# Optimization experiments

Measured on AMD Instinct MI355X. Metric: run time of the kernel, lower is better.

The kernel has to match this reference:

```python
import jax, jax.numpy as jnp
import numpy as np

EMBED_DIM = 1024
NUM_HEADS = 16
HEAD_DIM = EMBED_DIM // NUM_HEADS
LN_EPS = 1e-5


def setup_inputs() -> dict:
    key = jax.random.key(0)
    ks = jax.random.split(key, 12)
    B, SQ, SKV, E = 2, 1024, 4096, EMBED_DIM
    s = 1.0 / np.sqrt(E)
    return {
        "query": jax.random.normal(ks[0], (B, SQ, E), jnp.float32),
        "key_value": jax.random.normal(ks[1], (B, SKV, E), jnp.float32),
        "key_value_mask": jax.random.randint(ks[2], (B, SKV), 0, 2, jnp.int32),
        "Wq": jax.random.normal(ks[3], (E, E), jnp.float32) * s,
        "bq": jnp.zeros((E,), jnp.float32),
        "Wk": jax.random.normal(ks[4], (E, E), jnp.float32) * s,
        "bk": jnp.zeros((E,), jnp.float32),
        "Wv": jax.random.normal(ks[5], (E, E), jnp.float32) * s,
        "bv": jnp.zeros((E,), jnp.float32),
        "Wo": jax.random.normal(ks[6], (E, E), jnp.float32) * s,
        "bo": jnp.zeros((E,), jnp.float32),
        "ln_gamma": jnp.ones((E,), jnp.float32),
        "ln_beta": jnp.zeros((E,), jnp.float32),
    }


def reference(query, key_value, key_value_mask, Wq, bq, Wk, bk, Wv, bv, Wo, bo, ln_gamma, ln_beta):
    B, SQ, E = query.shape
    SKV = key_value.shape[1]
    H, D = NUM_HEADS, HEAD_DIM
    # projections (dropout is eval-mode identity)
    q = (query @ Wq.T + bq).reshape(B, SQ, H, D).transpose(0, 2, 1, 3)      # b h sq d
    k = (key_value @ Wk.T + bk).reshape(B, SKV, H, D).transpose(0, 2, 1, 3)  # b h skv d
    v = (key_value @ Wv.T + bv).reshape(B, SKV, H, D).transpose(0, 2, 1, 3)
    scale = jnp.sqrt(jnp.asarray(D, q.dtype))
    scores = jnp.einsum('bhqd,bhkd->bhqk', q, k) / scale                     # b h sq skv
    mask = (key_value_mask != 0)[:, None, None, :]                           # b 1 1 skv
    scores = jnp.where(mask, scores, jnp.asarray(-jnp.inf, scores.dtype))
    attn = jax.nn.softmax(scores, axis=-1)
    out = jnp.einsum('bhqk,bhkd->bhqd', attn, v)
    out = out.transpose(0, 2, 1, 3).reshape(B, SQ, E)
    out = out @ Wo.T + bo
    # post-LN residual
    x = query + out
    mu = jnp.mean(x, axis=-1, keepdims=True)
    var = jnp.mean(jnp.square(x - mu), axis=-1, keepdims=True)
    return (x - mu) * jax.lax.rsqrt(var + LN_EPS) * ln_gamma + ln_beta
```

## Files before the change

kernel.cpp:

```cpp
#include <hip/hip_runtime.h>
#include <cstdint>


typedef __bf16 bf16x8_t  __attribute__((ext_vector_type(8)));
typedef float  f32x4_t   __attribute__((ext_vector_type(4)));
typedef float  f32x16_t  __attribute__((ext_vector_type(16)));

#define E_DIM 1024
#define NH    16
#define HD    64
#define SCALE_L2E 0.1803368804f

__device__ __forceinline__ unsigned short f32_bf16(float f) {
    union { float f; unsigned int u; } v; v.f = f;
    unsigned int u = v.u;
    unsigned int r = (u + 0x7fffu + ((u >> 16) & 1u)) >> 16;
    return (unsigned short)r;
}

__device__ __forceinline__ unsigned pack_bf16(float a, float b) {
    __bf16 x = (__bf16)a, y = (__bf16)b;
    unsigned short ux = __builtin_bit_cast(unsigned short, x);
    unsigned short uy = __builtin_bit_cast(unsigned short, y);
    return (unsigned)ux | ((unsigned)uy << 16);
}

__device__ __forceinline__ void gld16(const unsigned short* g, unsigned short* l) {
    __builtin_amdgcn_global_load_lds(
        (const __attribute__((address_space(1))) unsigned int*)g,
        (__attribute__((address_space(3))) unsigned int*)l, 16, 0, 0);
}

__device__ __forceinline__ bf16x8_t ld16g(const unsigned short* p) {
    union { uint4 u; bf16x8_t f; } v;
    v.u = *reinterpret_cast<const uint4*>(p);
    return v.f;
}

__global__ void cast_all(const float* __restrict__ q, const float* __restrict__ kv,
                         const float* __restrict__ wq, const float* __restrict__ wk,
                         const float* __restrict__ wv, const float* __restrict__ wo,
                         unsigned short* __restrict__ Xq, unsigned short* __restrict__ Xkv,
                         unsigned short* __restrict__ Wqb, unsigned short* __restrict__ Wkb,
                         unsigned short* __restrict__ Wvb, unsigned short* __restrict__ Wob,
                         const int* __restrict__ msk, float* __restrict__ Sub) {
    __shared__ int red[4];
    if (blockIdx.x >= 14336) {
        int b = blockIdx.x - 14336, t = threadIdx.x;
        int s = 0;
#pragma unroll
        for (int k = 0; k < 16; k++) s += (msk[b * 4096 + k * 256 + t] != 0);
#pragma unroll
        for (int off = 32; off >= 1; off >>= 1) s += __shfl_xor(s, off, 64);
        if ((t & 63) == 0) red[t >> 6] = s;
        __syncthreads();
        if (t == 0)
            Sub[b] = (float)(4096 - (red[0] + red[1] + red[2] + red[3]));
        return;
    }
    long i = (long)blockIdx.x * 256 + threadIdx.x;
    const float* src; unsigned short* dst; long off;
    if (i < 2621440) {
        if (i < 524288) { src = q;  dst = Xq;  off = i; }
        else            { src = kv; dst = Xkv; off = i - 524288; }
    } else {
        long j = i - 2621440;
        int w = (int)(j >> 18); off = j & 262143;
        src = (w == 0) ? wq : (w == 1) ? wk : (w == 2) ? wv : wo;
        dst = (w == 0) ? Wqb : (w == 1) ? Wkb : (w == 2) ? Wvb : Wob;
    }
    float4 v = reinterpret_cast<const float4*>(src)[off];
    ushort4 o;
    o.x = f32_bf16(v.x); o.y = f32_bf16(v.y);
    o.z = f32_bf16(v.z); o.w = f32_bf16(v.w);
    reinterpret_cast<ushort4*>(dst)[off] = o;
}

#define BK 64

__global__ __launch_bounds__(256) void gemm_qkv(
    const unsigned short* __restrict__ Xq,
    const unsigned short* __restrict__ Xkv,
    const unsigned short* __restrict__ Wqb,
    const unsigned short* __restrict__ Wkb,
    const unsigned short* __restrict__ Wvb,
    const float* __restrict__ bq,
    const float* __restrict__ bk,
    const float* __restrict__ bv,
    unsigned short* __restrict__ Qout,
    unsigned short* __restrict__ Kout,
    unsigned short* __restrict__ Vout,
    const int* __restrict__ kvm)
{
    __shared__ __align__(16) unsigned short As[128 * BK];
    __shared__ __align__(16) unsigned short Bs[128 * BK];
    int bid  = blockIdx.x;
    int tid  = threadIdx.x;
    int lane = tid & 63;
    int wvu  = __builtin_amdgcn_readfirstlane(tid >> 6);
    int l15  = lane & 15, quad = lane >> 4, x7 = l15 & 7;

    if (bid < 1024) {
        int xcd  = bid & 7;
        int j    = bid >> 3;
        int mt   = xcd * 8 + (j >> 4);
        int sel  = j & 15;
        int isV  = sel >= 8;
        int m0   = mt * 128;
        int n0   = (sel & 7) * 128;
        const unsigned short* W = isV ? Wvb : Wkb;
        const float* bias = isV ? bv : bk;
        int wm   = ((tid >> 6) >> 1) * 64, wn = ((tid >> 6) & 1) * 64;

        f32x4_t acc[4][4];
#pragma unroll
        for (int i = 0; i < 4; i++)
#pragma unroll
            for (int jj = 0; jj < 4; jj++) acc[i][jj] = (f32x4_t)(0.f);

        for (int k0 = 0; k0 < 1024; k0 += BK) {
            __syncthreads();
#pragma unroll
            for (int i = 0; i < 4; i++) {
                int s = (i * 4 + wvu) * 64 + lane;
                int row = s >> 3, pcol = ((s & 7) ^ (row & 7)) << 3;
                gld16(&Xkv[(long)(m0 + row) * 1024 + k0 + pcol], &As[(i * 4 + wvu) * 512]);
                gld16(&W[(long)(n0 + row) * 1024 + k0 + pcol], &Bs[(i * 4 + wvu) * 512]);
            }
            __syncthreads();
            const char* Ab = (const char*)As;
            const char* Bb = (const char*)Bs;
#pragma unroll
            for (int ks = 0; ks < 2; ks++) {
                int pos = (((ks << 2) + quad) ^ x7) << 4;
                bf16x8_t af[4], bf[4];
#pragma unroll
                for (int mi = 0; mi < 4; mi++)
                    af[mi] = *reinterpret_cast<const bf16x8_t*>(
                        Ab + (wm + mi * 16 + l15) * 128 + pos);
#pragma unroll
                for (int ni = 0; ni < 4; ni++)
                    bf[ni] = *reinterpret_cast<const bf16x8_t*>(
                        Bb + (wn + ni * 16 + l15) * 128 + pos);
#pragma unroll
                for (int mi = 0; mi < 4; mi++)
#pragma unroll
                    for (int ni = 0; ni < 4; ni++)
                        acc[mi][ni] = __builtin_amdgcn_mfma_f32_16x16x32_bf16(
                            af[mi], bf[ni], acc[mi][ni], 0, 0, 0);
            }
        }
        int4 mk[4];
#pragma unroll
        for (int mi = 0; mi < 4; mi++) {
            int mg0 = m0 + wm + mi * 16 + quad * 4;
            mk[mi] = *reinterpret_cast<const int4*>(&kvm[mg0]);
        }
        if (!isV) {
#pragma unroll
            for (int mi = 0; mi < 4; mi++)
#pragma unroll
                for (int ni = 0; ni < 4; ni++) {
                    int n = n0 + wn + ni * 16 + l15;
                    float bvv = bias[n];
                    int h = n >> 6, d = n & 63;
#pragma unroll
                    for (int r = 0; r < 4; r++) {
                        int mg = m0 + wm + mi * 16 + quad * 4 + r;
                        int b = mg >> 12, s = mg & 4095;
                        unsigned short val = (&mk[mi].x)[r]
                            ? f32_bf16(acc[mi][ni][r] + bvv) : (unsigned short)0;
                        Kout[(((b * NH + h) << 12) + s) * HD + d] = val;
                    }
                }
        } else {
#pragma unroll
            for (int mi = 0; mi < 4; mi++)
#pragma unroll
                for (int ni = 0; ni < 4; ni++) {
                    int n = n0 + wn + ni * 16 + l15;
                    float bvv = bias[n];
                    int h = n >> 6, d = n & 63;
                    int mg0 = m0 + wm + mi * 16 + quad * 4;
                    int b = mg0 >> 12, s = mg0 & 4095;
                    ushort4 w;
                    w.x = mk[mi].x ? f32_bf16(acc[mi][ni][0] + bvv) : (unsigned short)0;
                    w.y = mk[mi].y ? f32_bf16(acc[mi][ni][1] + bvv) : (unsigned short)0;
                    w.z = mk[mi].z ? f32_bf16(acc[mi][ni][2] + bvv) : (unsigned short)0;
                    w.w = mk[mi].w ? f32_bf16(acc[mi][ni][3] + bvv) : (unsigned short)0;
                    *reinterpret_cast<ushort4*>(
                        &Vout[(((b * NH + h) * HD + d) << 12) + s]) = w;
                }
        }
    } else {
        int t    = bid - 1024;
        int xcd  = bid & 7;
        int j    = t >> 3;
        int mt   = xcd * 4 + (j >> 3);
        int m0   = mt * 64;
        int n0   = (j & 7) * 128;
        int wm   = ((tid >> 6) >> 1) * 32, wn = ((tid >> 6) & 1) * 64;

        f32x4_t acc[2][4];
#pragma unroll
        for (int i = 0; i < 2; i++)
#pragma unroll
            for (int jj = 0; jj < 4; jj++) acc[i][jj] = (f32x4_t)(0.f);

        for (int k0 = 0; k0 < 1024; k0 += BK) {
            __syncthreads();
#pragma unroll
            for (int i = 0; i < 2; i++) {
                int s = (i * 4 + wvu) * 64 + lane;
                int row = s >> 3, pcol = ((s & 7) ^ (row & 7)) << 3;
                gld16(&Xq[(long)(m0 + row) * 1024 + k0 + pcol], &As[(i * 4 + wvu) * 512]);
            }
#pragma unroll
            for (int i = 0; i < 4; i++) {
                int s = (i * 4 + wvu) * 64 + lane;
                int row = s >> 3, pcol = ((s & 7) ^ (row & 7)) << 3;
                gld16(&Wqb[(long)(n0 + row) * 1024 + k0 + pcol], &Bs[(i * 4 + wvu) * 512]);
            }
            __syncthreads();
            const char* Ab = (const char*)As;
            const char* Bb = (const char*)Bs;
#pragma unroll
            for (int ks = 0; ks < 2; ks++) {
                int pos = (((ks << 2) + quad) ^ x7) << 4;
                bf16x8_t af[2], bf[4];
#pragma unroll
                for (int mi = 0; mi < 2; mi++)
                    af[mi] = *reinterpret_cast<const bf16x8_t*>(
                        Ab + (wm + mi * 16 + l15) * 128 + pos);
#pragma unroll
                for (int ni = 0; ni < 4; ni++)
                    bf[ni] = *reinterpret_cast<const bf16x8_t*>(
                        Bb + (wn + ni * 16 + l15) * 128 + pos);
#pragma unroll
                for (int mi = 0; mi < 2; mi++)
#pragma unroll
                    for (int ni = 0; ni < 4; ni++)
                        acc[mi][ni] = __builtin_amdgcn_mfma_f32_16x16x32_bf16(
                            af[mi], bf[ni], acc[mi][ni], 0, 0, 0);
            }
        }
#pragma unroll
        for (int mi = 0; mi < 2; mi++)
#pragma unroll
            for (int ni = 0; ni < 4; ni++) {
                int n = n0 + wn + ni * 16 + l15;
                float bvq = bq[n];
                int h = n >> 6, d = n & 63;
#pragma unroll
                for (int r = 0; r < 4; r++) {
                    int mg = m0 + wm + mi * 16 + quad * 4 + r;
                    int b = mg >> 10, s = mg & 1023;
                    Qout[(((b * NH + h) << 10) + s) * HD + d] =
                        f32_bf16((acc[mi][ni][r] + bvq) * SCALE_L2E);
                }
            }
    }
}

__global__ __launch_bounds__(256) void gemm_oproj(
    const unsigned short* __restrict__ A,
    const unsigned short* __restrict__ W,
    const float* __restrict__ bias,
    const float* __restrict__ resid,
    float* __restrict__ xout)
{
    __shared__ __align__(16) unsigned short As[32 * BK];
    __shared__ __align__(16) unsigned short Bs[64 * BK];
    int tid  = threadIdx.x;
    int m0   = blockIdx.y * 32;
    int n0   = blockIdx.x * 64;
    int lane = tid & 63;
    int wvu  = __builtin_amdgcn_readfirstlane(tid >> 6);
    int l15  = lane & 15, quad = lane >> 4, x7 = l15 & 7;
    int wn   = (tid >> 6) * 16;

    f32x4_t acc[2];
    acc[0] = (f32x4_t)(0.f); acc[1] = (f32x4_t)(0.f);

    for (int k0 = 0; k0 < 1024; k0 += BK) {
        __syncthreads();
        {
            int s = wvu * 64 + lane;
            int row = s >> 3, pcol = ((s & 7) ^ (row & 7)) << 3;
            gld16(&A[(long)(m0 + row) * 1024 + k0 + pcol], &As[wvu * 512]);
        }
#pragma unroll
        for (int i = 0; i < 2; i++) {
            int s = (i * 4 + wvu) * 64 + lane;
            int row = s >> 3, pcol = ((s & 7) ^ (row & 7)) << 3;
            gld16(&W[(long)(n0 + row) * 1024 + k0 + pcol], &Bs[(i * 4 + wvu) * 512]);
        }
        __syncthreads();
        const char* Ab = (const char*)As;
        const char* Bb = (const char*)Bs;
#pragma unroll
        for (int ks = 0; ks < 2; ks++) {
            int pos = (((ks << 2) + quad) ^ x7) << 4;
            bf16x8_t af[2], bf;
#pragma unroll
            for (int mi = 0; mi < 2; mi++)
                af[mi] = *reinterpret_cast<const bf16x8_t*>(
                    Ab + (mi * 16 + l15) * 128 + pos);
            bf = *reinterpret_cast<const bf16x8_t*>(
                Bb + (wn + l15) * 128 + pos);
#pragma unroll
            for (int mi = 0; mi < 2; mi++)
                acc[mi] = __builtin_amdgcn_mfma_f32_16x16x32_bf16(
                    af[mi], bf, acc[mi], 0, 0, 0);
        }
    }
    int n = n0 + wn + l15;
    float bv = bias[n];
#pragma unroll
    for (int mi = 0; mi < 2; mi++)
#pragma unroll
        for (int r = 0; r < 4; r++) {
            int mg = m0 + mi * 16 + quad * 4 + r;
            xout[mg * 1024 + n] = acc[mi][r] + bv + resid[mg * 1024 + n];
        }
}

__global__ __launch_bounds__(512, 4) void attn_kernel(
    const unsigned short* __restrict__ Q,
    const unsigned short* __restrict__ K,
    const unsigned short* __restrict__ VT,
    float* __restrict__ Osc,
    float* __restrict__ Lsc)
{
    __shared__ __align__(16) union {
        struct { unsigned short Kb[2][4096]; unsigned short Vb[2][4096]; } st;
        struct { float OL[4][2048]; float ls[128]; } mg;
    } sm;

    int tid  = threadIdx.x;
    int lane = tid & 63;
    int w    = tid >> 6;
    int wvu  = __builtin_amdgcn_readfirstlane(w);
    int l31  = lane & 31, hw = lane >> 5;
    int qsub = w & 3, kvsub = w >> 2;

    int bid  = blockIdx.x;
    int xcd  = bid & 7, gidx = bid >> 3;
    int bh   = xcd * 4 + (gidx & 3);
    int rest = gidx >> 2;
    int q0   = (rest & 7) * 128;
    int bhalf = rest >> 3;

    const unsigned short* Kb = K + ((long)bh * 4096 + bhalf * 2048) * HD;
    const unsigned short* Vb = VT + (long)bh * HD * 4096 + bhalf * 2048;
    const unsigned short* Qb = Q + ((long)bh * 1024 + q0) * HD;

    bf16x8_t qfr[4];
#pragma unroll
    for (int ks = 0; ks < 4; ks++)
        qfr[ks] = ld16g(Qb + (qsub * 32 + l31) * HD + ks * 16 + hw * 8);

    f32x16_t oacc[2];
    oacc[0] = (f32x16_t)(0.f); oacc[1] = (f32x16_t)(0.f);
    float l_run = 0.f;

    auto stage = [&](int kt, int bufi) {
        int s = wvu * 64 + lane;
        int row = s >> 3, pc = ((s & 7) ^ (row & 7)) << 3;
        gld16(&Kb[(long)(kt * 64 + row) * HD + pc], &sm.st.Kb[bufi][wvu * 512]);
        gld16(&Vb[(long)row * 4096 + kt * 64 + pc], &sm.st.Vb[bufi][wvu * 512]);
    };

    const char* Kc = (const char*)sm.st.Kb;
    const char* Vc = (const char*)sm.st.Vb;

    stage(0, 0);
#pragma unroll 2
    for (int kt = 0; kt < 32; kt++) {
        __syncthreads();
        if (kt + 1 < 32) stage(kt + 1, (kt + 1) & 1);
        int bo = (kt & 1) * 8192;

        f32x16_t sa = (f32x16_t)(0.f);
        int krow = kvsub * 32 + l31;
        __builtin_amdgcn_s_setprio(1);
#pragma unroll
        for (int ks = 0; ks < 4; ks++) {
            int phys = (ks * 2 + hw) ^ (krow & 7);
            bf16x8_t kf = *reinterpret_cast<const bf16x8_t*>(
                Kc + bo + krow * 128 + phys * 16);
            sa = __builtin_amdgcn_mfma_f32_32x32x16_bf16(kf, qfr[ks], sa, 0, 0, 0);
        }
        __builtin_amdgcn_s_setprio(0);

        float pv[16];
#pragma unroll
        for (int r = 0; r < 16; r++) {
            float e;
            asm("v_exp_f32 %0, %1" : "=v"(e) : "v"(sa[r]));
            pv[r] = e;
        }
        float s0 = (pv[0] + pv[1]) + (pv[2] + pv[3]);
        float s1 = (pv[4] + pv[5]) + (pv[6] + pv[7]);
        float s2 = (pv[8] + pv[9]) + (pv[10] + pv[11]);
        float s3 = (pv[12] + pv[13]) + (pv[14] + pv[15]);
        l_run += (s0 + s1) + (s2 + s3);
        unsigned pku[8];
#pragma unroll
        for (int s4 = 0; s4 < 4; s4++) {
            pku[s4 * 2 + 0] = pack_bf16(pv[s4 * 4 + 0], pv[s4 * 4 + 1]);
            pku[s4 * 2 + 1] = pack_bf16(pv[s4 * 4 + 2], pv[s4 * 4 + 3]);
        }

        __builtin_amdgcn_s_setprio(1);
#pragma unroll
        for (int ks2 = 0; ks2 < 2; ks2++) {
            unsigned x0 = pku[(ks2 * 2) * 2 + 0];
            unsigned x1 = pku[(ks2 * 2) * 2 + 1];
            unsigned z0 = pku[(ks2 * 2 + 1) * 2 + 0];
            unsigned z1 = pku[(ks2 * 2 + 1) * 2 + 1];
            asm("v_permlane32_swap_b32 %0, %1" : "+v"(x0), "+v"(z0));
            asm("v_permlane32_swap_b32 %0, %1" : "+v"(x1), "+v"(z1));
            union { uint4 u; bf16x8_t f; } bw;
            bw.u.x = x0; bw.u.y = x1; bw.u.z = z0; bw.u.w = z1;
            int c = kvsub * 4 + ks2 * 2 + hw;
#pragma unroll
            for (int ds = 0; ds < 2; ds++) {
                int vrow = ds * 32 + l31;
                int phys = c ^ (vrow & 7);
                bf16x8_t va = *reinterpret_cast<const bf16x8_t*>(
                    Vc + bo + vrow * 128 + phys * 16);
                oacc[ds] = __builtin_amdgcn_mfma_f32_32x32x16_bf16(
                    va, bw.f, oacc[ds], 0, 0, 0);
            }
        }
        __builtin_amdgcn_s_setprio(0);
    }

    l_run += __shfl_xor(l_run, 32, 64);
    __syncthreads();
    if (kvsub == 1) {
        float* OL = sm.mg.OL[qsub];
#pragma unroll
        for (int ds = 0; ds < 2; ds++)
#pragma unroll
            for (int r = 0; r < 16; r++) {
                int d = ds * 32 + (r & 3) + 8 * (r >> 2) + 4 * hw;
                OL[d * 32 + l31] = oacc[ds][r];
            }
        if (hw == 0) sm.mg.ls[qsub * 32 + l31] = l_run;
    }
    __syncthreads();
    if (kvsub == 0) {
        const float* OL = sm.mg.OL[qsub];
        int q = q0 + qsub * 32 + l31;
        long obase = (((long)bhalf * 32 + bh) * 64) * 1024;
#pragma unroll
        for (int ds = 0; ds < 2; ds++)
#pragma unroll
            for (int r = 0; r < 16; r++) {
                int d = ds * 32 + (r & 3) + 8 * (r >> 2) + 4 * hw;
                Osc[obase + (long)d * 1024 + q] = oacc[ds][r] + OL[d * 32 + l31];
            }
        if (hw == 0)
            Lsc[((long)bhalf * 32 + bh) * 1024 + q] = l_run + sm.mg.ls[qsub * 32 + l31];
    }
}

__global__ __launch_bounds__(256) void attn_merge(
    const float* __restrict__ Osc, const float* __restrict__ Lsc,
    const float* __restrict__ Sub, unsigned short* __restrict__ AO)
{
    __shared__ unsigned short T[64 * 66];
    int t = threadIdx.x, w = t >> 6, lane = t & 63;
    int bh = blockIdx.y, b = bh >> 4, h = bh & 15;
    int q0 = blockIdx.x * 64;
    int q = q0 + lane;

    float ls = Lsc[(long)bh * 1024 + q]
             + Lsc[(long)(32 + bh) * 1024 + q] - Sub[b];
    float inv = __builtin_amdgcn_rcpf(ls);
    inv = inv * (2.f - ls * inv);

#pragma unroll
    for (int dd = 0; dd < 16; dd++) {
        int d = w * 16 + dd;
        long base = (long)bh * 64 * 1024 + (long)d * 1024 + q;
        float o = Osc[base] + Osc[base + 32l * 64 * 1024];
        T[lane * 66 + d] = f32_bf16(o * inv);
    }
    __syncthreads();
    int q2 = t >> 2, c16 = (t & 3) * 16;
    unsigned ov[8];
#pragma unroll
    for (int j = 0; j < 8; j++)
        ov[j] = *reinterpret_cast<const unsigned*>(&T[q2 * 66 + c16 + j * 2]);
    unsigned short* dst = &AO[((long)(b * 1024 + q0 + q2)) * E_DIM + h * HD + c16];
    reinterpret_cast<uint4*>(dst)[0] = make_uint4(ov[0], ov[1], ov[2], ov[3]);
    reinterpret_cast<uint4*>(dst)[1] = make_uint4(ov[4], ov[5], ov[6], ov[7]);
}

__global__ __launch_bounds__(256) void ln_kernel(
    const float* __restrict__ x, const float* __restrict__ g,
    const float* __restrict__ be, float* __restrict__ out)
{
    __shared__ float red[8];
    int row = blockIdx.x, tid = threadIdx.x;
    float4 v = reinterpret_cast<const float4*>(x)[row * 256 + tid];
    float s  = v.x + v.y + v.z + v.w;
    float sq = v.x * v.x + v.y * v.y + v.z * v.z + v.w * v.w;
#pragma unroll
    for (int off = 32; off >= 1; off >>= 1) {
        s  += __shfl_xor(s,  off, 64);
        sq += __shfl_xor(sq, off, 64);
    }
    if ((tid & 63) == 0) { red[tid >> 6] = s; red[4 + (tid >> 6)] = sq; }
    __syncthreads();
    s  = red[0] + red[1] + red[2] + red[3];
    sq = red[4] + red[5] + red[6] + red[7];
    float mu  = s * (1.f / 1024.f);
    float var = sq * (1.f / 1024.f) - mu * mu;
    float rs  = rsqrtf(var + 1e-5f);
    int c = tid * 4;
    float4 o;
    o.x = (v.x - mu) * rs * g[c]     + be[c];
    o.y = (v.y - mu) * rs * g[c + 1] + be[c + 1];
    o.z = (v.z - mu) * rs * g[c + 2] + be[c + 2];
    o.w = (v.w - mu) * rs * g[c + 3] + be[c + 3];
    reinterpret_cast<float4*>(out)[row * 256 + tid] = o;
}

extern "C" void kernel_launch(void* const* d_in, const int* in_sizes, int n_in,
                              void* d_out, int out_size, void* d_ws, size_t ws_size,
                              hipStream_t stream) {
    const float* query     = (const float*)d_in[0];
    const float* key_value = (const float*)d_in[1];
    const int*   kv_mask   = (const int*)d_in[2];
    const float* Wq = (const float*)d_in[3];
    const float* bq = (const float*)d_in[4];
    const float* Wk = (const float*)d_in[5];
    const float* bk = (const float*)d_in[6];
    const float* Wv = (const float*)d_in[7];
    const float* bv = (const float*)d_in[8];
    const float* Wo = (const float*)d_in[9];
    const float* bo = (const float*)d_in[10];
    const float* ln_g = (const float*)d_in[11];
    const float* ln_b = (const float*)d_in[12];
    float* out = (float*)d_out;

    char* ws = (char*)d_ws;
    unsigned short* Xq  = (unsigned short*)(ws);
    unsigned short* Xkv = (unsigned short*)(ws + (4ll  << 20));
    unsigned short* Wqb = (unsigned short*)(ws + (20ll << 20));
    unsigned short* Wkb = (unsigned short*)(ws + (22ll << 20));
    unsigned short* Wvb = (unsigned short*)(ws + (24ll << 20));
    float*          Osc = (float*)(ws);
    unsigned short* Kh  = (unsigned short*)(ws + (32ll << 20));
    unsigned short* VTh = (unsigned short*)(ws + (48ll << 20));
    unsigned short* AO  = (unsigned short*)(ws + (64ll << 20));
    float*          Xr  = (float*)(ws + (68ll << 20));
    float*          Lsc = (float*)(ws + (76ll << 20));
    float*          Sub = (float*)(ws + (77ll << 20));
    unsigned short* Qh  = (unsigned short*)(ws + (80ll << 20));
    unsigned short* Wob = (unsigned short*)(ws + (84ll << 20));

    cast_all<<<14338, 256, 0, stream>>>(query, key_value, Wq, Wk, Wv, Wo,
                                        Xq, Xkv, Wqb, Wkb, Wvb, Wob,
                                        kv_mask, Sub);

    gemm_qkv<<<1280, 256, 0, stream>>>(Xq, Xkv, Wqb, Wkb, Wvb, bq, bk, bv,
                                       Qh, Kh, VTh, kv_mask);

    attn_kernel<<<512, 512, 0, stream>>>(Qh, Kh, VTh, Osc, Lsc);
    attn_merge<<<dim3(16, 32), 256, 0, stream>>>(Osc, Lsc, Sub, AO);

    gemm_oproj<<<dim3(16, 64), 256, 0, stream>>>(AO, Wob, bo, query, Xr);

    ln_kernel<<<2048, 256, 0, stream>>>(Xr, ln_g, ln_b, out);
}
```

Baseline: 231.1 us.

## Fuse K and V projections per block to reuse shared activation tile

Each K/V GEMM block now computes both the K and V outputs for the same 128x128 tile, loading the Xkv activation tile into shared memory once and reusing it for both weight matrices. This halves the K/V block count and removes redundant activation loads from global memory. In exchange, accumulator registers double (two 4x4 f32x4 sets) and LDS use grows to three tiles. That can lower occupancy or cause spills, and with fewer blocks per launch wave balance may be worse.

Result: slower. 252.1 us (+9.1%).

```diff
diff --git a/kernel.cpp b/kernel.cpp
--- a/kernel.cpp
+++ b/kernel.cpp
@@ -93,30 +93,30 @@
     const int* __restrict__ kvm)
 {
     __shared__ __align__(16) unsigned short As[128 * BK];
-    __shared__ __align__(16) unsigned short Bs[128 * BK];
+    __shared__ __align__(16) unsigned short Bsk[128 * BK];
+    __shared__ __align__(16) unsigned short Bsv[128 * BK];
     int bid  = blockIdx.x;
     int tid  = threadIdx.x;
     int lane = tid & 63;
     int wvu  = __builtin_amdgcn_readfirstlane(tid >> 6);
     int l15  = lane & 15, quad = lane >> 4, x7 = l15 & 7;
 
-    if (bid < 1024) {
+    if (bid < 512) {
         int xcd  = bid & 7;
         int j    = bid >> 3;
-        int mt   = xcd * 8 + (j >> 4);
-        int sel  = j & 15;
-        int isV  = sel >= 8;
+        int mt   = xcd * 8 + (j >> 3);
         int m0   = mt * 128;
-        int n0   = (sel & 7) * 128;
-        const unsigned short* W = isV ? Wvb : Wkb;
-        const float* bias = isV ? bv : bk;
+        int n0   = (j & 7) * 128;
         int wm   = ((tid >> 6) >> 1) * 64, wn = ((tid >> 6) & 1) * 64;
 
-        f32x4_t acc[4][4];
+        f32x4_t ak[4][4], av[4][4];
 #pragma unroll
         for (int i = 0; i < 4; i++)
 #pragma unroll
-            for (int jj = 0; jj < 4; jj++) acc[i][jj] = (f32x4_t)(0.f);
+            for (int jj = 0; jj < 4; jj++) {
+                ak[i][jj] = (f32x4_t)(0.f);
+                av[i][jj] = (f32x4_t)(0.f);
+            }
 
         for (int k0 = 0; k0 < 1024; k0 += BK) {
             __syncthreads();
@@ -125,29 +125,37 @@
                 int s = (i * 4 + wvu) * 64 + lane;
                 int row = s >> 3, pcol = ((s & 7) ^ (row & 7)) << 3;
                 gld16(&Xkv[(long)(m0 + row) * 1024 + k0 + pcol], &As[(i * 4 + wvu) * 512]);
-                gld16(&W[(long)(n0 + row) * 1024 + k0 + pcol], &Bs[(i * 4 + wvu) * 512]);
+                gld16(&Wkb[(long)(n0 + row) * 1024 + k0 + pcol], &Bsk[(i * 4 + wvu) * 512]);
+                gld16(&Wvb[(long)(n0 + row) * 1024 + k0 + pcol], &Bsv[(i * 4 + wvu) * 512]);
             }
             __syncthreads();
             const char* Ab = (const char*)As;
-            const char* Bb = (const char*)Bs;
+            const char* Kb = (const char*)Bsk;
+            const char* Vb = (const char*)Bsv;
 #pragma unroll
             for (int ks = 0; ks < 2; ks++) {
                 int pos = (((ks << 2) + quad) ^ x7) << 4;
-                bf16x8_t af[4], bf[4];
+                bf16x8_t af[4], bfk[4], bfv[4];
 #pragma unroll
                 for (int mi = 0; mi < 4; mi++)
                     af[mi] = *reinterpret_cast<const bf16x8_t*>(
                         Ab + (wm + mi * 16 + l15) * 128 + pos);
 #pragma unroll
-                for (int ni = 0; ni < 4; ni++)
-                    bf[ni] = *reinterpret_cast<const bf16x8_t*>(
-                        Bb + (wn + ni * 16 + l15) * 128 + pos);
+                for (int ni = 0; ni < 4; ni++) {
+                    bfk[ni] = *reinterpret_cast<const bf16x8_t*>(
+                        Kb + (wn + ni * 16 + l15) * 128 + pos);
+                    bfv[ni] = *reinterpret_cast<const bf16x8_t*>(
+                        Vb + (wn + ni * 16 + l15) * 128 + pos);
+                }
 #pragma unroll
                 for (int mi = 0; mi < 4; mi++)
 #pragma unroll
-                    for (int ni = 0; ni < 4; ni++)
-                        acc[mi][ni] = __builtin_amdgcn_mfma_f32_16x16x32_bf16(
-                            af[mi], bf[ni], acc[mi][ni], 0, 0, 0);
+                    for (int ni = 0; ni < 4; ni++) {
+                        ak[mi][ni] = __builtin_amdgcn_mfma_f32_16x16x32_bf16(
+                            af[mi], bfk[ni], ak[mi][ni], 0, 0, 0);
+                        av[mi][ni] = __builtin_amdgcn_mfma_f32_16x16x32_bf16(
+                            af[mi], bfv[ni], av[mi][ni], 0, 0, 0);
+                    }
             }
         }
         int4 mk[4];
@@ -156,45 +164,42 @@
             int mg0 = m0 + wm + mi * 16 + quad * 4;
             mk[mi] = *reinterpret_cast<const int4*>(&kvm[mg0]);
         }
-        if (!isV) {
-#pragma unroll
-            for (int mi = 0; mi < 4; mi++)
-#pragma unroll
-                for (int ni = 0; ni < 4; ni++) {
-                    int n = n0 + wn + ni * 16 + l15;
-                    float bvv = bias[n];
-                    int h = n >> 6, d = n & 63;
-#pragma unroll
-                    for (int r = 0; r < 4; r++) {
-                        int mg = m0 + wm + mi * 16 + quad * 4 + r;
-                        int b = mg >> 12, s = mg & 4095;
-                        unsigned short val = (&mk[mi].x)[r]
-                            ? f32_bf16(acc[mi][ni][r] + bvv) : (unsigned short)0;
-                        Kout[(((b * NH + h) << 12) + s) * HD + d] = val;
-                    }
+#pragma unroll
+        for (int mi = 0; mi < 4; mi++)
+#pragma unroll
+            for (int ni = 0; ni < 4; ni++) {
+                int n = n0 + wn + ni * 16 + l15;
+                float bkk = bk[n];
+                int h = n >> 6, d = n & 63;
+#pragma unroll
+                for (int r = 0; r < 4; r++) {
+                    int mg = m0 + wm + mi * 16 + quad * 4 + r;
+                    int b = mg >> 12, s = mg & 4095;
+                    unsigned short val = (&mk[mi].x)[r]
+                        ? f32_bf16(ak[mi][ni][r] + bkk) : (unsigned short)0;
+                    Kout[(((b * NH + h) << 12) + s) * HD + d] = val;
                 }
-        } else {
-#pragma unroll
-            for (int mi = 0; mi < 4; mi++)
-#pragma unroll
-                for (int ni = 0; ni < 4; ni++) {
-                    int n = n0 + wn + ni * 16 + l15;
-                    float bvv = bias[n];
-                    int h = n >> 6, d = n & 63;
-                    int mg0 = m0 + wm + mi * 16 + quad * 4;
-                    int b = mg0 >> 12, s = mg0 & 4095;
-                    ushort4 w;
-                    w.x = mk[mi].x ? f32_bf16(acc[mi][ni][0] + bvv) : (unsigned short)0;
-                    w.y = mk[mi].y ? f32_bf16(acc[mi][ni][1] + bvv) : (unsigned short)0;
-                    w.z = mk[mi].z ? f32_bf16(acc[mi][ni][2] + bvv) : (unsigned short)0;
-                    w.w = mk[mi].w ? f32_bf16(acc[mi][ni][3] + bvv) : (unsigned short)0;
-                    *reinterpret_cast<ushort4*>(
-                        &Vout[(((b * NH + h) * HD + d) << 12) + s]) = w;
-                }
-        }
+            }
+#pragma unroll
+        for (int mi = 0; mi < 4; mi++)
+#pragma unroll
+            for (int ni = 0; ni < 4; ni++) {
+                int n = n0 + wn + ni * 16 + l15;
+                float bvv = bv[n];
+                int h = n >> 6, d = n & 63;
+                int mg0 = m0 + wm + mi * 16 + quad * 4;
+                int b = mg0 >> 12, s = mg0 & 4095;
+                ushort4 w;
+                w.x = mk[mi].x ? f32_bf16(av[mi][ni][0] + bvv) : (unsigned short)0;
+                w.y = mk[mi].y ? f32_bf16(av[mi][ni][1] + bvv) : (unsigned short)0;
+                w.z = mk[mi].z ? f32_bf16(av[mi][ni][2] + bvv) : (unsigned short)0;
+                w.w = mk[mi].w ? f32_bf16(av[mi][ni][3] + bvv) : (unsigned short)0;
+                *reinterpret_cast<ushort4*>(
+                    &Vout[(((b * NH + h) * HD + d) << 12) + s]) = w;
+            }
     } else {
-        int t    = bid - 1024;
-        int xcd  = bid & 7;
+        int t    = bid - 512;
+        int xcd  = t & 7;
         int j    = t >> 3;
         int mt   = xcd * 4 + (j >> 3);
         int m0   = mt * 64;
@@ -219,11 +224,11 @@
             for (int i = 0; i < 4; i++) {
                 int s = (i * 4 + wvu) * 64 + lane;
                 int row = s >> 3, pcol = ((s & 7) ^ (row & 7)) << 3;
-                gld16(&Wqb[(long)(n0 + row) * 1024 + k0 + pcol], &Bs[(i * 4 + wvu) * 512]);
+                gld16(&Wqb[(long)(n0 + row) * 1024 + k0 + pcol], &Bsk[(i * 4 + wvu) * 512]);
             }
             __syncthreads();
             const char* Ab = (const char*)As;
-            const char* Bb = (const char*)Bs;
+            const char* Bb = (const char*)Bsk;
 #pragma unroll
             for (int ks = 0; ks < 2; ks++) {
                 int pos = (((ks << 2) + quad) ^ x7) << 4;
@@ -568,8 +573,8 @@
                                         Xq, Xkv, Wqb, Wkb, Wvb, Wob,
                                         kv_mask, Sub);
 
-    gemm_qkv<<<1280, 256, 0, stream>>>(Xq, Xkv, Wqb, Wkb, Wvb, bq, bk, bv,
-                                       Qh, Kh, VTh, kv_mask);
+    gemm_qkv<<<768, 256, 0, stream>>>(Xq, Xkv, Wqb, Wkb, Wvb, bq, bk, bv,
+                                      Qh, Kh, VTh, kv_mask);
 
     attn_kernel<<<512, 512, 0, stream>>>(Qh, Kh, VTh, Osc, Lsc);
     attn_merge<<<dim3(16, 32), 256, 0, stream>>>(Osc, Lsc, Sub, AO);
```
